# Kernel optimization log

Measured on AMD Instinct MI355X. Metric: run time of the kernel, lower is better.

## Reference

```python
import jax, jax.numpy as jnp
import numpy as np

B, T, C = 2, 2048, 1024
NH = 16
HD = C // NH

def build_alibi_bias(n_head, max_len):
    slopes = jnp.arange(1, n_head + 1, dtype=jnp.float32) / n_head  # [nh]
    ar = jnp.arange(max_len, dtype=jnp.float32)
    # bias[h, i, j] = slopes[h] * (j - i)
    return slopes[:, None, None] * (ar[None, None, :] - ar[None, :, None])

def setup_inputs() -> dict:
    key = jax.random.key(0)
    ks = jax.random.split(key, 7)
    s = 0.02
    return {
        "x": jax.random.normal(ks[0], (B, T, C), dtype=jnp.float32),
        "q_w": jax.random.normal(ks[1], (C, C), dtype=jnp.float32) * s,   # [in, out]
        "q_b": jnp.zeros((C,), dtype=jnp.float32),
        "kv_w": jax.random.normal(ks[2], (C, 2 * C), dtype=jnp.float32) * s,
        "kv_b": jnp.zeros((2 * C,), dtype=jnp.float32),
        "o_w": jax.random.normal(ks[3], (C, C), dtype=jnp.float32) * s,
        "o_b": jnp.zeros((C,), dtype=jnp.float32),
    }

def reference(x, q_w, q_b, kv_w, kv_b, o_w, o_b):
    Bx, Tx, Cx = x.shape
    q = (x @ q_w + q_b).reshape(Bx, Tx, NH, HD).transpose(0, 2, 1, 3)      # [B,nh,T,hd]
    kv = (x @ kv_w + kv_b).reshape(Bx, Tx, 2, NH, HD).transpose(2, 0, 3, 1, 4)
    k, v = kv[0], kv[1]                                                     # [B,nh,T,hd]
    att = jnp.einsum("bhqd,bhkd->bhqk", q, k) * (1.0 / np.sqrt(HD))        # [B,nh,T,T]
    att = att + build_alibi_bias(NH, Tx)[None]                              # ALiBi bias
    causal = jnp.tril(jnp.ones((Tx, Tx), dtype=bool))
    att = jnp.where(causal[None, None], att, -jnp.inf)
    att = jax.nn.softmax(att, axis=-1)
    y = jnp.einsum("bhqk,bhkd->bhqd", att, v)                               # [B,nh,T,hd]
    y = y.transpose(0, 2, 1, 3).reshape(Bx, Tx, Cx)
    return y @ o_w + o_b
```

## Files before the change

kernel.cpp:

```cpp
#include <hip/hip_runtime.h>
#include <hip/hip_bf16.h>

#define NB 2
#define NT 2048
#define NC 1024
#define NHD 16
#define HDD 64
#define LOG2E 1.4426950408889634f

typedef __attribute__((ext_vector_type(8))) short short8;
typedef __attribute__((ext_vector_type(4))) float f32x4;

__device__ __forceinline__ ushort f2bf(float f) {
    union { float f; unsigned u; } v; v.f = f;
    unsigned u = v.u;
    unsigned r = (u + 0x7FFFu + ((u >> 16) & 1u)) >> 16;
    return (ushort)r;
}

__global__ __launch_bounds__(256)
void cvtx(const float* __restrict__ src, ushort* __restrict__ dst, int n)
{
    int i = (blockIdx.x * 256 + threadIdx.x) * 8;
    if (i >= n) return;
    float4 a = *(const float4*)(src + i);
    float4 b = *(const float4*)(src + i + 4);
    short8 o;
    o[0] = (short)f2bf(a.x); o[1] = (short)f2bf(a.y);
    o[2] = (short)f2bf(a.z); o[3] = (short)f2bf(a.w);
    o[4] = (short)f2bf(b.x); o[5] = (short)f2bf(b.y);
    o[6] = (short)f2bf(b.z); o[7] = (short)f2bf(b.w);
    *(short8*)(dst + i) = o;
}

__global__ __launch_bounds__(256)
void tcvt(const float* __restrict__ src, ushort* __restrict__ dst, int Kd, int Nd)
{
    __shared__ ushort tile[64][68];
    const int tid = threadIdx.x;
    const int kb = blockIdx.x * 64, nb = blockIdx.y * 64;
    const int r = tid >> 2, c = (tid & 3) * 16;
    const float* sp = src + (size_t)(kb + r) * Nd + nb + c;
#pragma unroll
    for (int i = 0; i < 16; i += 4) {
        float4 v = *(const float4*)(sp + i);
        tile[r][c + i + 0] = f2bf(v.x);
        tile[r][c + i + 1] = f2bf(v.y);
        tile[r][c + i + 2] = f2bf(v.z);
        tile[r][c + i + 3] = f2bf(v.w);
    }
    __syncthreads();
    ushort* dp = dst + (size_t)(nb + r) * Kd + kb + c;
#pragma unroll
    for (int i = 0; i < 16; i += 8) {
        short8 o;
#pragma unroll
        for (int j = 0; j < 8; j++) o[j] = (short)tile[c + i + j][r];
        *(short8*)(dp + i) = o;
    }
}

__global__ __launch_bounds__(256)
void vtr(const ushort* __restrict__ src, ushort* __restrict__ dst)
{
    __shared__ ushort tile[64][66];
    const int tid = threadIdx.x;
    const int bh = blockIdx.y;
    const int t0 = blockIdx.x * 64;
    const int r = tid >> 2, c = (tid & 3) * 16;
    const ushort* sp = src + ((size_t)bh * NT + t0 + r) * HDD + c;
    *(short8*)&tile[r][c]     = *(const short8*)sp;
    *(short8*)&tile[r][c + 8] = *(const short8*)(sp + 8);
    __syncthreads();
    ushort* dp = dst + ((size_t)bh * HDD + r) * NT + t0 + c;
    short8 o0, o1;
#pragma unroll
    for (int j = 0; j < 8; j++) { o0[j] = (short)tile[c + j][r]; o1[j] = (short)tile[c + 8 + j][r]; }
    *(short8*)dp = o0;
    *(short8*)(dp + 8) = o1;
}

template<int MODE>
__global__ __launch_bounds__(256)
void gemm128(const ushort* __restrict__ A, const ushort* __restrict__ Bt,
             const float* __restrict__ bias0, const float* __restrict__ bias1,
             ushort* __restrict__ Qo, ushort* __restrict__ Ko, ushort* __restrict__ Vo,
             float* __restrict__ Fo, int Kdim)
{
    __shared__ ushort Al[128][40];
    __shared__ ushort Bl[128][40];
    const int tid = threadIdx.x;
    const int lane = tid & 63, w = tid >> 6;
    const int wr = (w >> 1) * 64, wc = (w & 1) * 64;
    const int lg = lane >> 4, lc = lane & 15;
    const int bm = blockIdx.x * 128, bn = blockIdx.y * 128;

    f32x4 acc[4][4] = {};

    const int r = tid >> 1, cs = (tid & 1) * 16;
    const ushort* ap = A + (size_t)(bm + r) * Kdim + cs;
    const ushort* bp = Bt + (size_t)(bn + r) * Kdim + cs;

    for (int k0 = 0; k0 < Kdim; k0 += 32) {
        __syncthreads();
        *(short8*)&Al[r][cs]     = *(const short8*)(ap + k0);
        *(short8*)&Al[r][cs + 8] = *(const short8*)(ap + k0 + 8);
        *(short8*)&Bl[r][cs]     = *(const short8*)(bp + k0);
        *(short8*)&Bl[r][cs + 8] = *(const short8*)(bp + k0 + 8);
        __syncthreads();
        short8 af[4], bfv[4];
#pragma unroll
        for (int mt = 0; mt < 4; mt++) af[mt] = *(const short8*)&Al[wr + mt*16 + lc][lg*8];
#pragma unroll
        for (int nt = 0; nt < 4; nt++) bfv[nt] = *(const short8*)&Bl[wc + nt*16 + lc][lg*8];
#pragma unroll
        for (int mt = 0; mt < 4; mt++)
#pragma unroll
            for (int nt = 0; nt < 4; nt++)
                acc[mt][nt] = __builtin_amdgcn_mfma_f32_16x16x32_bf16(af[mt], bfv[nt], acc[mt][nt], 0, 0, 0);
    }

#pragma unroll
    for (int mt = 0; mt < 4; mt++) {
#pragma unroll
        for (int nt = 0; nt < 4; nt++) {
#pragma unroll
            for (int rr = 0; rr < 4; rr++) {
                int m = bm + wr + mt*16 + lg*4 + rr;
                int n = bn + wc + nt*16 + lc;
                float v = acc[mt][nt][rr];
                if (MODE == 0) {
                    int b = m >> 11, t = m & 2047;
                    if (n < NC) {
                        float q = (v + bias0[n]) * (0.125f * LOG2E);
                        int hh = n >> 6, d = n & 63;
                        Qo[(((size_t)b*NHD + hh)*NT + t)*HDD + d] = f2bf(q);
                    } else {
                        int j = n - NC;
                        float val = v + bias1[j];
                        int s = j >> 10;
                        int jj = j & 1023;
                        int hh = jj >> 6, d = jj & 63;
                        ushort* dst = s ? Vo : Ko;
                        dst[(((size_t)b*NHD + hh)*NT + t)*HDD + d] = f2bf(val);
                    }
                } else {
                    Fo[(size_t)m * NC + n] = v + bias0[n];
                }
            }
        }
    }
}

__global__ __launch_bounds__(256)
void attn_fwd(const ushort* __restrict__ Q, const ushort* __restrict__ K,
              const ushort* __restrict__ Vt, ushort* __restrict__ Y)
{
    __shared__ ushort Kl[64][72];
    __shared__ ushort Vl[64][72];
    __shared__ ushort Pl[4][16][72];

    const int tid = threadIdx.x;
    const int lane = tid & 63, w = tid >> 6;
    const int lg = lane >> 4, lc = lane & 15;
    const int qt = 31 - (blockIdx.x >> 5);
    const int bh = blockIdx.x & 31;
    const int b = bh >> 4, h = bh & 15;

    const ushort* Qp = Q + (size_t)bh * NT * HDD;
    const ushort* Kp = K + (size_t)bh * NT * HDD;
    const ushort* Vp = Vt + (size_t)bh * HDD * NT;

    const float slope2 = (float)(h + 1) * (LOG2E / (float)NHD);
    const int sr = tid >> 2, sd = (tid & 3) * 16;
    const float alk0 = slope2 * (float)lc;
    const float s16 = slope2 * 16.0f;

    short8 ones;
#pragma unroll
    for (int j = 0; j < 8; j++) ones[j] = (short)0x3F80;

    const int q0 = qt * 64 + w * 16;
    short8 qf0, qf1;
    {
        const ushort* qr = Qp + (size_t)(q0 + lc) * HDD + lg * 8;
        qf0 = *(const short8*)qr;
        qf1 = *(const short8*)(qr + 32);
    }
    float m_i[4], l_i[4], sc[4];
    f32x4 acc[4] = {};
#pragma unroll
    for (int r4 = 0; r4 < 4; r4++) { m_i[r4] = -1e30f; l_i[r4] = 0.f; }

    const int ntile = qt + 1;

    short8 pk0, pk1, pv0, pv1;
    {
        const ushort* kp = Kp + (size_t)sr * HDD + sd;
        pk0 = *(const short8*)kp;
        pk1 = *(const short8*)(kp + 8);
        const ushort* vp = Vp + (size_t)sr * NT + sd;
        pv0 = *(const short8*)vp;
        pv1 = *(const short8*)(vp + 8);
    }

    for (int t0 = 0; t0 < ntile; t0++) {
        const int kv0 = t0 * 64;
        __syncthreads();
        *(short8*)&Kl[sr][sd]     = pk0;
        *(short8*)&Kl[sr][sd + 8] = pk1;
        *(short8*)&Vl[sr][sd]     = pv0;
        *(short8*)&Vl[sr][sd + 8] = pv1;
        __syncthreads();

        if (t0 + 1 < ntile) {
            const int kv1 = kv0 + 64;
            const ushort* kp = Kp + (size_t)(kv1 + sr) * HDD + sd;
            pk0 = *(const short8*)kp;
            pk1 = *(const short8*)(kp + 8);
            const ushort* vp = Vp + (size_t)sr * NT + kv1 + sd;
            pv0 = *(const short8*)vp;
            pv1 = *(const short8*)(vp + 8);
        }

        f32x4 s[4];
#pragma unroll
        for (int kt = 0; kt < 4; kt++) {
            short8 kf0 = *(const short8*)&Kl[kt*16 + lc][lg*8];
            short8 kf1 = *(const short8*)&Kl[kt*16 + lc][32 + lg*8];
            f32x4 z = {0.f, 0.f, 0.f, 0.f};
            z = __builtin_amdgcn_mfma_f32_16x16x32_bf16(qf0, kf0, z, 0, 0, 0);
            s[kt] = __builtin_amdgcn_mfma_f32_16x16x32_bf16(qf1, kf1, z, 0, 0, 0);
        }

        float bk[4];
        bk[0] = slope2 * (float)kv0 + alk0;
        bk[1] = bk[0] + s16; bk[2] = bk[1] + s16; bk[3] = bk[2] + s16;

        const bool diag = (t0 == qt);
#pragma unroll
        for (int rr = 0; rr < 4; rr++) {
            float x[4];
#pragma unroll
            for (int kt = 0; kt < 4; kt++) x[kt] = s[kt][rr] + bk[kt];
            if (diag) {
                const int qi = q0 + lg*4 + rr;
#pragma unroll
                for (int kt = 0; kt < 4; kt++) {
                    int kj = kv0 + kt*16 + lc;
                    x[kt] = (kj > qi) ? -1e30f : x[kt];
                }
            }
            float rmax = fmaxf(fmaxf(x[0], x[1]), fmaxf(x[2], x[3]));
#pragma unroll
            for (int mm = 1; mm < 16; mm <<= 1) rmax = fmaxf(rmax, __shfl_xor(rmax, mm));
            if (rmax - m_i[rr] > 8.0f) {
                float mn = fmaxf(m_i[rr], rmax);
                sc[rr] = exp2f(m_i[rr] - mn);
                m_i[rr] = mn;
            } else {
                sc[rr] = 1.0f;
            }
#pragma unroll
            for (int kt = 0; kt < 4; kt++) {
                float pv = exp2f(x[kt] - m_i[rr]);
                unsigned pb; __builtin_memcpy(&pb, &pv, 4);
                Pl[w][lg*4 + rr][kt*16 + lc] = (ushort)(pb >> 16);
            }
        }
        if (__any(sc[0] != 1.0f || sc[1] != 1.0f || sc[2] != 1.0f || sc[3] != 1.0f)) {
#pragma unroll
            for (int dt = 0; dt < 4; dt++)
#pragma unroll
                for (int rr = 0; rr < 4; rr++) acc[dt][rr] *= sc[rr];
        }

        short8 pa0 = *(const short8*)&Pl[w][lc][lg*8];
        short8 pa1 = *(const short8*)&Pl[w][lc][32 + lg*8];

        f32x4 rsv = {0.f, 0.f, 0.f, 0.f};
        rsv = __builtin_amdgcn_mfma_f32_16x16x32_bf16(pa0, ones, rsv, 0, 0, 0);
        rsv = __builtin_amdgcn_mfma_f32_16x16x32_bf16(pa1, ones, rsv, 0, 0, 0);

#pragma unroll
        for (int dt = 0; dt < 4; dt++) {
            short8 vb0 = *(const short8*)&Vl[dt*16 + lc][lg*8];
            short8 vb1 = *(const short8*)&Vl[dt*16 + lc][32 + lg*8];
            acc[dt] = __builtin_amdgcn_mfma_f32_16x16x32_bf16(pa0, vb0, acc[dt], 0, 0, 0);
            acc[dt] = __builtin_amdgcn_mfma_f32_16x16x32_bf16(pa1, vb1, acc[dt], 0, 0, 0);
        }
#pragma unroll
        for (int rr = 0; rr < 4; rr++) l_i[rr] = l_i[rr] * sc[rr] + rsv[rr];
    }

    float inv[4];
#pragma unroll
    for (int rr = 0; rr < 4; rr++) inv[rr] = __builtin_amdgcn_rcpf(l_i[rr]);
#pragma unroll
    for (int dt = 0; dt < 4; dt++) {
#pragma unroll
        for (int rr = 0; rr < 4; rr++) {
            int t = q0 + lg*4 + rr;
            int d = dt*16 + lc;
            Y[((size_t)b * NT + t) * NC + h * HDD + d] = f2bf(acc[dt][rr] * inv[rr]);
        }
    }
}

extern "C" void kernel_launch(void* const* d_in, const int* in_sizes, int n_in,
                              void* d_out, int out_size, void* d_ws, size_t ws_size,
                              hipStream_t stream)
{
    const float* x    = (const float*)d_in[0];
    const float* q_w  = (const float*)d_in[1];
    const float* q_b  = (const float*)d_in[2];
    const float* kv_w = (const float*)d_in[3];
    const float* kv_b = (const float*)d_in[4];
    const float* o_w  = (const float*)d_in[5];
    const float* o_b  = (const float*)d_in[6];
    float* out = (float*)d_out;

    char* ws = (char*)d_ws;
    ushort* xb    = (ushort*)(ws);
    ushort* wqkvT = (ushort*)(ws + 8388608);
    ushort* woT   = (ushort*)(ws + 14680064);
    ushort* Qs    = (ushort*)(ws + 16777216);
    ushort* Ks    = (ushort*)(ws + 25165824);
    ushort* Vs    = (ushort*)(ws + 33554432);
    ushort* Ys    = (ushort*)(ws + 41943040);
    ushort* VsT   = xb;

    cvtx<<<2048, 256, 0, stream>>>(x, xb, NB*NT*NC);
    tcvt<<<dim3(16,16), 256, 0, stream>>>(q_w, wqkvT, 1024, 1024);
    tcvt<<<dim3(16,32), 256, 0, stream>>>(kv_w, wqkvT + 1024*1024, 1024, 2048);
    tcvt<<<dim3(16,16), 256, 0, stream>>>(o_w, woT, 1024, 1024);
    gemm128<0><<<dim3(32,24), 256, 0, stream>>>(xb, wqkvT, q_b, kv_b, Qs, Ks, Vs, nullptr, 1024);
    vtr<<<dim3(32,32), 256, 0, stream>>>(Vs, VsT);
    attn_fwd<<<1024, 256, 0, stream>>>(Qs, Ks, VsT, Ys);
    gemm128<1><<<dim3(32,8), 256, 0, stream>>>(Ys, woT, o_b, nullptr, nullptr, nullptr, nullptr, out, 1024);
}
```

Baseline: 162.4 us.

## Rewrite attention with 32x32 MFMA, register-resident P, and direct-to-LDS GEMM loads

```diff
diff --git a/kernel.cpp b/kernel.cpp
--- a/kernel.cpp
+++ b/kernel.cpp
@@ -10,12 +10,23 @@
 
 typedef __attribute__((ext_vector_type(8))) short short8;
 typedef __attribute__((ext_vector_type(4))) float f32x4;
+typedef __attribute__((ext_vector_type(16))) float f32x16;
 
 __device__ __forceinline__ ushort f2bf(float f) {
     union { float f; unsigned u; } v; v.f = f;
     unsigned u = v.u;
     unsigned r = (u + 0x7FFFu + ((u >> 16) & 1u)) >> 16;
     return (ushort)r;
+}
+
+__device__ __forceinline__ unsigned pkbf(float a, float b) {
+    __hip_bfloat162 t = __float22bfloat162_rn(float2{a, b});
+    unsigned u; __builtin_memcpy(&u, &t, 4); return u;
+}
+
+__device__ __forceinline__ void gload16(const ushort* g, ushort* l) {
+    __builtin_amdgcn_global_load_lds((const __attribute__((address_space(1))) void*)g,
+                                     (__attribute__((address_space(3))) void*)l, 16, 0, 0);
 }
 
 __global__ __launch_bounds__(256)
@@ -87,8 +98,8 @@
              ushort* __restrict__ Qo, ushort* __restrict__ Ko, ushort* __restrict__ Vo,
              float* __restrict__ Fo, int Kdim)
 {
-    __shared__ ushort Al[128][40];
-    __shared__ ushort Bl[128][40];
+    __shared__ ushort Al[128 * 32];
+    __shared__ ushort Bl[128 * 32];
     const int tid = threadIdx.x;
     const int lane = tid & 63, w = tid >> 6;
     const int wr = (w >> 1) * 64, wc = (w & 1) * 64;
@@ -97,22 +108,23 @@
 
     f32x4 acc[4][4] = {};
 
-    const int r = tid >> 1, cs = (tid & 1) * 16;
-    const ushort* ap = A + (size_t)(bm + r) * Kdim + cs;
-    const ushort* bp = Bt + (size_t)(bn + r) * Kdim + cs;
+    const int srow = lane >> 2, scol = (lane & 3) * 8;
 
     for (int k0 = 0; k0 < Kdim; k0 += 32) {
         __syncthreads();
-        *(short8*)&Al[r][cs]     = *(const short8*)(ap + k0);
-        *(short8*)&Al[r][cs + 8] = *(const short8*)(ap + k0 + 8);
-        *(short8*)&Bl[r][cs]     = *(const short8*)(bp + k0);
-        *(short8*)&Bl[r][cs + 8] = *(const short8*)(bp + k0 + 8);
+#pragma unroll
+        for (int c = 0; c < 2; c++) {
+            int seg = w * 2 + c;
+            int row = seg * 16 + srow;
+            gload16(A  + (size_t)(bm + row) * Kdim + k0 + scol, &Al[seg * 512]);
+            gload16(Bt + (size_t)(bn + row) * Kdim + k0 + scol, &Bl[seg * 512]);
+        }
         __syncthreads();
         short8 af[4], bfv[4];
 #pragma unroll
-        for (int mt = 0; mt < 4; mt++) af[mt] = *(const short8*)&Al[wr + mt*16 + lc][lg*8];
-#pragma unroll
-        for (int nt = 0; nt < 4; nt++) bfv[nt] = *(const short8*)&Bl[wc + nt*16 + lc][lg*8];
+        for (int mt = 0; mt < 4; mt++) af[mt] = *(const short8*)&Al[(wr + mt*16 + lc) * 32 + lg*8];
+#pragma unroll
+        for (int nt = 0; nt < 4; nt++) bfv[nt] = *(const short8*)&Bl[(wc + nt*16 + lc) * 32 + lg*8];
 #pragma unroll
         for (int mt = 0; mt < 4; mt++)
 #pragma unroll
@@ -152,18 +164,18 @@
     }
 }
 
-__global__ __launch_bounds__(256)
+__global__ __launch_bounds__(256, 3)
 void attn_fwd(const ushort* __restrict__ Q, const ushort* __restrict__ K,
               const ushort* __restrict__ Vt, ushort* __restrict__ Y)
 {
-    __shared__ ushort Kl[64][72];
-    __shared__ ushort Vl[64][72];
-    __shared__ ushort Pl[4][16][72];
+    __shared__ ushort sb[2 * 64 * 72];
+    ushort* Kl = sb;
+    ushort* Vl = sb + 64 * 72;
 
     const int tid = threadIdx.x;
     const int lane = tid & 63, w = tid >> 6;
-    const int lg = lane >> 4, lc = lane & 15;
-    const int qt = 31 - (blockIdx.x >> 5);
+    const int lo5 = lane & 31, hi = lane >> 5;
+    const int qt = 15 - (int)(blockIdx.x >> 5);
     const int bh = blockIdx.x & 31;
     const int b = bh >> 4, h = bh & 15;
 
@@ -171,28 +183,31 @@
     const ushort* Kp = K + (size_t)bh * NT * HDD;
     const ushort* Vp = Vt + (size_t)bh * HDD * NT;
 
+    const int bq0 = qt * 128;
+    const int q0 = bq0 + w * 32;
+    const int qlane = q0 + lo5;
+
     const float slope2 = (float)(h + 1) * (LOG2E / (float)NHD);
+
+    short8 qf[4];
+    {
+        const ushort* qr = Qp + (size_t)qlane * HDD + 8 * hi;
+#pragma unroll
+        for (int kk = 0; kk < 4; kk++) qf[kk] = *(const short8*)(qr + kk * 16);
+    }
+
+    float bb[16];
+#pragma unroll
+    for (int r = 0; r < 16; r++) {
+        int roff = (r & 3) + 8 * (r >> 2) + 4 * hi;
+        bb[r] = slope2 * ((float)roff - (float)qlane);
+    }
+
+    float m_s = -1e30f, l_s = 0.f;
+    f32x16 accO[2] = {};
+
+    const int ntile = 2 * qt + 2;
     const int sr = tid >> 2, sd = (tid & 3) * 16;
-    const float alk0 = slope2 * (float)lc;
-    const float s16 = slope2 * 16.0f;
-
-    short8 ones;
-#pragma unroll
-    for (int j = 0; j < 8; j++) ones[j] = (short)0x3F80;
-
-    const int q0 = qt * 64 + w * 16;
-    short8 qf0, qf1;
-    {
-        const ushort* qr = Qp + (size_t)(q0 + lc) * HDD + lg * 8;
-        qf0 = *(const short8*)qr;
-        qf1 = *(const short8*)(qr + 32);
-    }
-    float m_i[4], l_i[4], sc[4];
-    f32x4 acc[4] = {};
-#pragma unroll
-    for (int r4 = 0; r4 < 4; r4++) { m_i[r4] = -1e30f; l_i[r4] = 0.f; }
-
-    const int ntile = qt + 1;
 
     short8 pk0, pk1, pv0, pv1;
     {
@@ -204,16 +219,16 @@
         pv1 = *(const short8*)(vp + 8);
     }
 
-    for (int t0 = 0; t0 < ntile; t0++) {
-        const int kv0 = t0 * 64;
+    for (int t = 0; t < ntile; t++) {
+        const int kv0 = t * 64;
         __syncthreads();
-        *(short8*)&Kl[sr][sd]     = pk0;
-        *(short8*)&Kl[sr][sd + 8] = pk1;
-        *(short8*)&Vl[sr][sd]     = pv0;
-        *(short8*)&Vl[sr][sd + 8] = pv1;
+        *(short8*)&Kl[sr * 72 + sd]     = pk0;
+        *(short8*)&Kl[sr * 72 + sd + 8] = pk1;
+        *(short8*)&Vl[sr * 72 + sd]     = pv0;
+        *(short8*)&Vl[sr * 72 + sd + 8] = pv1;
         __syncthreads();
 
-        if (t0 + 1 < ntile) {
+        if (t + 1 < ntile) {
             const int kv1 = kv0 + 64;
             const ushort* kp = Kp + (size_t)(kv1 + sr) * HDD + sd;
             pk0 = *(const short8*)kp;
@@ -223,88 +238,100 @@
             pv1 = *(const short8*)(vp + 8);
         }
 
-        f32x4 s[4];
-#pragma unroll
-        for (int kt = 0; kt < 4; kt++) {
-            short8 kf0 = *(const short8*)&Kl[kt*16 + lc][lg*8];
-            short8 kf1 = *(const short8*)&Kl[kt*16 + lc][32 + lg*8];
-            f32x4 z = {0.f, 0.f, 0.f, 0.f};
-            z = __builtin_amdgcn_mfma_f32_16x16x32_bf16(qf0, kf0, z, 0, 0, 0);
-            s[kt] = __builtin_amdgcn_mfma_f32_16x16x32_bf16(qf1, kf1, z, 0, 0, 0);
-        }
-
-        float bk[4];
-        bk[0] = slope2 * (float)kv0 + alk0;
-        bk[1] = bk[0] + s16; bk[2] = bk[1] + s16; bk[3] = bk[2] + s16;
-
-        const bool diag = (t0 == qt);
-#pragma unroll
-        for (int rr = 0; rr < 4; rr++) {
-            float x[4];
-#pragma unroll
-            for (int kt = 0; kt < 4; kt++) x[kt] = s[kt][rr] + bk[kt];
-            if (diag) {
-                const int qi = q0 + lg*4 + rr;
-#pragma unroll
-                for (int kt = 0; kt < 4; kt++) {
-                    int kj = kv0 + kt*16 + lc;
-                    x[kt] = (kj > qi) ? -1e30f : x[kt];
+#pragma unroll
+        for (int sub = 0; sub < 2; sub++) {
+            const int kv0s = kv0 + sub * 32;
+            if (kv0s > q0 + 31) continue;
+
+            f32x16 S = {};
+#pragma unroll
+            for (int kk = 0; kk < 4; kk++) {
+                short8 kf = *(const short8*)&Kl[(sub * 32 + lo5) * 72 + kk * 16 + 8 * hi];
+                S = __builtin_amdgcn_mfma_f32_32x32x16_bf16(kf, qf[kk], S, 0, 0, 0);
+            }
+
+            const float sk = slope2 * (float)kv0s;
+            float mloc = m_s - sk;
+
+            if (kv0s + 31 > q0) {
+#pragma unroll
+                for (int r = 0; r < 16; r++) {
+                    int kvr = kv0s + (r & 3) + 8 * (r >> 2) + 4 * hi;
+                    S[r] = (kvr > qlane) ? -1e30f : (S[r] + bb[r]);
                 }
-            }
-            float rmax = fmaxf(fmaxf(x[0], x[1]), fmaxf(x[2], x[3]));
-#pragma unroll
-            for (int mm = 1; mm < 16; mm <<= 1) rmax = fmaxf(rmax, __shfl_xor(rmax, mm));
-            if (rmax - m_i[rr] > 8.0f) {
-                float mn = fmaxf(m_i[rr], rmax);
-                sc[rr] = exp2f(m_i[rr] - mn);
-                m_i[rr] = mn;
             } else {
-                sc[rr] = 1.0f;
-            }
-#pragma unroll
-            for (int kt = 0; kt < 4; kt++) {
-                float pv = exp2f(x[kt] - m_i[rr]);
-                unsigned pb; __builtin_memcpy(&pb, &pv, 4);
-                Pl[w][lg*4 + rr][kt*16 + lc] = (ushort)(pb >> 16);
-            }
-        }
-        if (__any(sc[0] != 1.0f || sc[1] != 1.0f || sc[2] != 1.0f || sc[3] != 1.0f)) {
-#pragma unroll
-            for (int dt = 0; dt < 4; dt++)
-#pragma unroll
-                for (int rr = 0; rr < 4; rr++) acc[dt][rr] *= sc[rr];
-        }
-
-        short8 pa0 = *(const short8*)&Pl[w][lc][lg*8];
-        short8 pa1 = *(const short8*)&Pl[w][lc][32 + lg*8];
-
-        f32x4 rsv = {0.f, 0.f, 0.f, 0.f};
-        rsv = __builtin_amdgcn_mfma_f32_16x16x32_bf16(pa0, ones, rsv, 0, 0, 0);
-        rsv = __builtin_amdgcn_mfma_f32_16x16x32_bf16(pa1, ones, rsv, 0, 0, 0);
-
-#pragma unroll
-        for (int dt = 0; dt < 4; dt++) {
-            short8 vb0 = *(const short8*)&Vl[dt*16 + lc][lg*8];
-            short8 vb1 = *(const short8*)&Vl[dt*16 + lc][32 + lg*8];
-            acc[dt] = __builtin_amdgcn_mfma_f32_16x16x32_bf16(pa0, vb0, acc[dt], 0, 0, 0);
-            acc[dt] = __builtin_amdgcn_mfma_f32_16x16x32_bf16(pa1, vb1, acc[dt], 0, 0, 0);
-        }
-#pragma unroll
-        for (int rr = 0; rr < 4; rr++) l_i[rr] = l_i[rr] * sc[rr] + rsv[rr];
-    }
-
-    float inv[4];
-#pragma unroll
-    for (int rr = 0; rr < 4; rr++) inv[rr] = __builtin_amdgcn_rcpf(l_i[rr]);
-#pragma unroll
-    for (int dt = 0; dt < 4; dt++) {
-#pragma unroll
-        for (int rr = 0; rr < 4; rr++) {
-            int t = q0 + lg*4 + rr;
-            int d = dt*16 + lc;
-            Y[((size_t)b * NT + t) * NC + h * HDD + d] = f2bf(acc[dt][rr] * inv[rr]);
-        }
-    }
+#pragma unroll
+                for (int r = 0; r < 16; r++) S[r] = S[r] + bb[r];
+            }
+
+            float rmax = S[0];
+#pragma unroll
+            for (int r = 1; r < 16; r++) rmax = fmaxf(rmax, S[r]);
+            rmax = fmaxf(rmax, __shfl_xor(rmax, 32));
+
+            if (__any(rmax - mloc > 8.0f)) {
+                float mn = fmaxf(mloc, rmax);
+                float sc = __builtin_amdgcn_exp2f(mloc - mn);
+                mloc = mn;
+                l_s *= sc;
+#pragma unroll
+                for (int dt = 0; dt < 2; dt++)
+#pragma unroll
+                    for (int r = 0; r < 16; r++) accO[dt][r] *= sc;
+            }
+            m_s = mloc + sk;
+
+            float p[16], sum = 0.f;
+#pragma unroll
+            for (int r = 0; r < 16; r++) {
+                p[r] = __builtin_amdgcn_exp2f(S[r] - mloc);
+                sum += p[r];
+            }
+            sum += __shfl_xor(sum, 32);
+            l_s += sum;
+
+            unsigned pw[8], px[8];
+#pragma unroll
+            for (int i = 0; i < 8; i++) pw[i] = pkbf(p[2 * i], p[2 * i + 1]);
+#pragma unroll
+            for (int i = 0; i < 8; i++) px[i] = __shfl_xor(pw[i], 32);
+            union { unsigned u[4]; short8 s; } fa0, fa1;
+            fa0.u[0] = hi ? px[2] : pw[0];
+            fa0.u[1] = hi ? px[3] : pw[1];
+            fa0.u[2] = hi ? pw[2] : px[0];
+            fa0.u[3] = hi ? pw[3] : px[1];
+            fa1.u[0] = hi ? px[6] : pw[4];
+            fa1.u[1] = hi ? px[7] : pw[5];
+            fa1.u[2] = hi ? pw[6] : px[4];
+            fa1.u[3] = hi ? pw[7] : px[5];
+
+#pragma unroll
+            for (int dt = 0; dt < 2; dt++) {
+                short8 vf0 = *(const short8*)&Vl[(dt * 32 + lo5) * 72 + sub * 32 + 8 * hi];
+                short8 vf1 = *(const short8*)&Vl[(dt * 32 + lo5) * 72 + sub * 32 + 16 + 8 * hi];
+                accO[dt] = __builtin_amdgcn_mfma_f32_32x32x16_bf16(vf0, fa0.s, accO[dt], 0, 0, 0);
+                accO[dt] = __builtin_amdgcn_mfma_f32_32x32x16_bf16(vf1, fa1.s, accO[dt], 0, 0, 0);
+            }
+        }
+    }
+
+    const float invl = __builtin_amdgcn_rcpf(l_s);
+    __syncthreads();
+    ushort* myO = sb + w * 32 * 72;
+#pragma unroll
+    for (int dt = 0; dt < 2; dt++)
+#pragma unroll
+        for (int r = 0; r < 16; r++) {
+            int d = dt * 32 + (r & 3) + 8 * (r >> 2) + 4 * hi;
+            myO[lo5 * 72 + d] = f2bf(accO[dt][r] * invl);
+        }
+    __syncthreads();
+    const int orow = lane >> 1, ocol = (lane & 1) * 32;
+    const int qg = q0 + orow;
+    ushort* yp = Y + ((size_t)b * NT + qg) * NC + h * HDD + ocol;
+#pragma unroll
+    for (int c = 0; c < 4; c++)
+        *(short8*)(yp + c * 8) = *(const short8*)&myO[orow * 72 + ocol + c * 8];
 }
 
 extern "C" void kernel_launch(void* const* d_in, const int* in_sizes, int n_in,
@@ -336,6 +363,6 @@
     tcvt<<<dim3(16,16), 256, 0, stream>>>(o_w, woT, 1024, 1024);
     gemm128<0><<<dim3(32,24), 256, 0, stream>>>(xb, wqkvT, q_b, kv_b, Qs, Ks, Vs, nullptr, 1024);
     vtr<<<dim3(32,32), 256, 0, stream>>>(Vs, VsT);
-    attn_fwd<<<1024, 256, 0, stream>>>(Qs, Ks, VsT, Ys);
+    attn_fwd<<<512, 256, 0, stream>>>(Qs, Ks, VsT, Ys);
     gemm128<1><<<dim3(32,8), 256, 0, stream>>>(Ys, woT, o_b, nullptr, nullptr, nullptr, nullptr, out, 1024);
 }
```

Result: faster. 150.2 us (-7.5%).
